# Performance work log

Measured on AMD Instinct MI355X. Metric: run time of the kernel, lower is better.

Reference implementation:

```python
import jax, jax.numpy as jnp
import numpy as np

LSTM_H = 4

def spp(x):
    # x: (N, C, H, W) -> (N, C*5) via adaptive max pool at levels [2, 1]
    N, C, H, W = x.shape
    p2 = x.reshape(N, C, 2, H // 2, 2, W // 2).max(axis=(3, 5)).reshape(N, C * 4)
    p1 = x.max(axis=(2, 3))  # (N, C)
    return jnp.concatenate([p2, p1], axis=1)  # (N, 15)

def setup_inputs() -> dict:
    key = jax.random.key(0)
    ks = jax.random.split(key, 12)
    B, S, C, H, W = 16, 128, 3, 224, 224
    s = 0.1
    return {
        "frames": jax.random.normal(ks[0], (B, S, C, H, W), dtype=jnp.float32),
        "Wf": jax.random.normal(ks[1], (15, 15), dtype=jnp.float32) * s,
        "bf": jax.random.normal(ks[2], (15,), dtype=jnp.float32) * s,
        "We": jax.random.normal(ks[3], (8, 15), dtype=jnp.float32) * s,
        "be": jax.random.normal(ks[4], (8,), dtype=jnp.float32) * s,
        "Wih": jax.random.normal(ks[5], (4 * LSTM_H, 8), dtype=jnp.float32) * s,
        "Whh": jax.random.normal(ks[6], (4 * LSTM_H, LSTM_H), dtype=jnp.float32) * s,
        "bih": jax.random.normal(ks[7], (4 * LSTM_H,), dtype=jnp.float32) * s,
        "bhh": jax.random.normal(ks[8], (4 * LSTM_H,), dtype=jnp.float32) * s,
        "Wp": jax.random.normal(ks[9], (1, LSTM_H), dtype=jnp.float32) * s,
        "bp": jax.random.normal(ks[10], (1,), dtype=jnp.float32) * s,
    }

def _lstm_cell(x, h, c, Wih, Whh, bih, bhh):
    gates = x @ Wih.T + h @ Whh.T + bih + bhh  # (B, 4H)
    i, f, g, o = jnp.split(gates, 4, axis=-1)  # torch gate order: i, f, g, o
    c2 = jax.nn.sigmoid(f) * c + jax.nn.sigmoid(i) * jnp.tanh(g)
    h2 = jax.nn.sigmoid(o) * jnp.tanh(c2)
    return h2, c2

def reference(frames, Wf, bf, We, be, Wih, Whh, bih, bhh, Wp, bp):
    B, S, C, H, W = frames.shape
    pooled_flat = spp(frames.reshape(B * S, C, H, W))          # (B*S, 15)
    forecasted_flat = pooled_flat @ Wf.T + bf                   # (B*S, 15)
    pooled = pooled_flat.reshape(B, S, 15)
    forecasted_pooled = forecasted_flat.reshape(B, S, 15)

    emb = pooled @ We.T + be                 # (B, S, 8)
    femb = forecasted_pooled @ We.T + be     # (B, S, 8)

    def step(carry, xs):
        h, c = carry
        e_t, fe_t = xs                       # each (B, 8)
        h1, c1 = _lstm_cell(e_t, h, c, Wih, Whh, bih, bhh)
        h2, _ = _lstm_cell(fe_t, h1, c1, Wih, Whh, bih, bhh)
        return (h1, c1), (h1, h2)

    h0 = jnp.zeros((B, LSTM_H), dtype=frames.dtype)
    c0 = jnp.zeros((B, LSTM_H), dtype=frames.dtype)
    xs = (jnp.swapaxes(emb, 0, 1), jnp.swapaxes(femb, 0, 1))   # (S, B, 8)
    _, (hs, fhs) = jax.lax.scan(step, (h0, c0), xs)            # (S, B, 4)

    progress = jax.nn.sigmoid(hs @ Wp.T + bp)[..., 0].T        # (B, S)
    forecasted_progress = jax.nn.sigmoid(fhs @ Wp.T + bp)[..., 0].T
    return (progress, forecasted_progress, pooled, forecasted_pooled)
```

## Files before the change

kernel.cpp:

```cpp
#include <hip/hip_runtime.h>
#include <math.h>

#define NEGINF (-INFINITY)

typedef float fvec4 __attribute__((ext_vector_type(4)));

template <int M>
__device__ __forceinline__ float qbcast(float v) {
    return __int_as_float(
        __builtin_amdgcn_update_dpp(0, __float_as_int(v), M * 0x55, 0xF, 0xF, true));
}
__device__ __forceinline__ float fsigmoid(float z) { return 1.f / (1.f + __expf(-z)); }
__device__ __forceinline__ float ftanh(float z) {
    z = fminf(fmaxf(z, -20.f), 20.f);
    float e = __expf(2.f * z);
    return (e - 1.f) / (e + 1.f);
}

__global__ __launch_bounds__(448, 7) void spp_prep_kernel(
    const float* __restrict__ frames, const float* __restrict__ Wf,
    const float* __restrict__ bf, const float* __restrict__ We,
    const float* __restrict__ be, float* __restrict__ out_pooled,
    float* __restrict__ out_fc, float* __restrict__ emb,
    float* __restrict__ femb) {
    int n = blockIdx.x;
    int tid = threadIdx.x;
    const fvec4* __restrict__ base =
        reinterpret_cast<const fvec4*>(frames) + (size_t)n * 37632;
    int cc = tid % 56;
    bool left = cc < 28;

    __shared__ float sred[7][4];
    __shared__ float sq[3][4];
    __shared__ float sp[15], sfc[15];

    for (int c = 0; c < 3; ++c) {
        const fvec4* __restrict__ p = base + c * 12544 + tid;
        float aT = NEGINF, aB = NEGINF;
#pragma unroll 7
        for (int r = 0; r < 14; ++r) {
            fvec4 f = __builtin_nontemporal_load(&p[r * 448]);
            aT = fmaxf(aT, fmaxf(fmaxf(f.x, f.y), fmaxf(f.z, f.w)));
        }
#pragma unroll 7
        for (int r = 14; r < 28; ++r) {
            fvec4 f = __builtin_nontemporal_load(&p[r * 448]);
            aB = fmaxf(aB, fmaxf(fmaxf(f.x, f.y), fmaxf(f.z, f.w)));
        }
        float tl = left ? aT : NEGINF;
        float tr = left ? NEGINF : aT;
        float bl = left ? aB : NEGINF;
        float br = left ? NEGINF : aB;
#pragma unroll
        for (int m = 32; m >= 1; m >>= 1) {
            tl = fmaxf(tl, __shfl_xor(tl, m, 64));
            tr = fmaxf(tr, __shfl_xor(tr, m, 64));
            bl = fmaxf(bl, __shfl_xor(bl, m, 64));
            br = fmaxf(br, __shfl_xor(br, m, 64));
        }
        int w = tid >> 6;
        if ((tid & 63) == 0) { sred[w][0] = tl; sred[w][1] = tr; sred[w][2] = bl; sred[w][3] = br; }
        __syncthreads();
        if (tid < 4) {
            float v = sred[0][tid];
#pragma unroll
            for (int ww = 1; ww < 7; ++ww) v = fmaxf(v, sred[ww][tid]);
            sq[c][tid] = v;
        }
        __syncthreads();
    }

    if (tid < 12) {
        sp[tid] = ((const float*)sq)[tid];
    } else if (tid >= 16 && tid < 19) {
        int c = tid - 16;
        sp[12 + c] = fmaxf(fmaxf(sq[c][0], sq[c][1]), fmaxf(sq[c][2], sq[c][3]));
    }
    __syncthreads();
    if (tid < 15) {
        float a = bf[tid];
#pragma unroll
        for (int kk = 0; kk < 15; ++kk) a += sp[kk] * Wf[tid * 15 + kk];
        sfc[tid] = a;
        out_pooled[n * 15 + tid] = sp[tid];
        out_fc[n * 15 + tid] = a;
    }
    __syncthreads();
    if (tid < 8) {
        float a = be[tid], a2 = be[tid];
#pragma unroll
        for (int kk = 0; kk < 15; ++kk) {
            a  += sp[kk]  * We[tid * 15 + kk];
            a2 += sfc[kk] * We[tid * 15 + kk];
        }
        emb[n * 8 + tid]  = a;
        femb[n * 8 + tid] = a2;
    }
}

__device__ __forceinline__ float dot8(const float4& a, const float4& b,
                                      const float* __restrict__ w) {
    return a.x * w[0] + a.y * w[1] + a.z * w[2] + a.w * w[3] +
           b.x * w[4] + b.y * w[5] + b.z * w[6] + b.w * w[7];
}

__global__ __launch_bounds__(64) void lstm_kernel(
    const float* __restrict__ emb, const float* __restrict__ femb,
    const float* __restrict__ Wih, const float* __restrict__ Whh,
    const float* __restrict__ bih, const float* __restrict__ bhh,
    const float* __restrict__ Wp, const float* __restrict__ bp,
    float* __restrict__ prog, float* __restrict__ fprog) {
    int tid = threadIdx.x;
    int b = tid >> 2, k = tid & 3;
    float wih[4][8], whh[4][4], bsum[4];
#pragma unroll
    for (int g = 0; g < 4; g++) {
        int row = g * 4 + k;
#pragma unroll
        for (int m = 0; m < 8; m++) wih[g][m] = Wih[row * 8 + m];
#pragma unroll
        for (int m = 0; m < 4; m++) whh[g][m] = Whh[row * 4 + m];
        bsum[g] = bih[row] + bhh[row];
    }
    float wpv[4];
#pragma unroll
    for (int m = 0; m < 4; m++) wpv[m] = Wp[m];
    float bpv = bp[0];

    const float* xe = emb  + b * 1024;
    const float* xf = femb + b * 1024;

    float xd1[4], xd2[4];
    {
        float4 a0 = *(const float4*)(xe);
        float4 a1 = *(const float4*)(xe + 4);
        float4 f0 = *(const float4*)(xf);
        float4 f1 = *(const float4*)(xf + 4);
#pragma unroll
        for (int g = 0; g < 4; g++) {
            xd1[g] = bsum[g] + dot8(a0, a1, wih[g]);
            xd2[g] = bsum[g] + dot8(f0, f1, wih[g]);
        }
    }

    float h0 = 0.f, h1r = 0.f, h2r = 0.f, h3r = 0.f;
    float ck = 0.f;

    for (int s2 = 0; s2 < 128; ++s2) {
        int sn = (s2 < 127) ? s2 + 1 : 127;
        float4 na0 = *(const float4*)(xe + sn * 8);
        float4 na1 = *(const float4*)(xe + sn * 8 + 4);
        float4 nf0 = *(const float4*)(xf + sn * 8);
        float4 nf1 = *(const float4*)(xf + sn * 8 + 4);

        float g0 = xd1[0] + h0 * whh[0][0] + h1r * whh[0][1] + h2r * whh[0][2] + h3r * whh[0][3];
        float g1 = xd1[1] + h0 * whh[1][0] + h1r * whh[1][1] + h2r * whh[1][2] + h3r * whh[1][3];
        float g2 = xd1[2] + h0 * whh[2][0] + h1r * whh[2][1] + h2r * whh[2][2] + h3r * whh[2][3];
        float g3 = xd1[3] + h0 * whh[3][0] + h1r * whh[3][1] + h2r * whh[3][2] + h3r * whh[3][3];
        float c1  = fsigmoid(g1) * ck + fsigmoid(g0) * ftanh(g2);
        float hk1 = fsigmoid(g3) * ftanh(c1);
        float b0 = qbcast<0>(hk1), b1 = qbcast<1>(hk1), b2 = qbcast<2>(hk1), b3 = qbcast<3>(hk1);
        float z = bpv + b0 * wpv[0] + b1 * wpv[1] + b2 * wpv[2] + b3 * wpv[3];
        if (k == 0) prog[b * 128 + s2] = fsigmoid(z);

        float e0 = xd2[0] + b0 * whh[0][0] + b1 * whh[0][1] + b2 * whh[0][2] + b3 * whh[0][3];
        float e1 = xd2[1] + b0 * whh[1][0] + b1 * whh[1][1] + b2 * whh[1][2] + b3 * whh[1][3];
        float e2 = xd2[2] + b0 * whh[2][0] + b1 * whh[2][1] + b2 * whh[2][2] + b3 * whh[2][3];
        float e3 = xd2[3] + b0 * whh[3][0] + b1 * whh[3][1] + b2 * whh[3][2] + b3 * whh[3][3];
        float c2v = fsigmoid(e1) * c1 + fsigmoid(e0) * ftanh(e2);
        float hk2 = fsigmoid(e3) * ftanh(c2v);
        float d0 = qbcast<0>(hk2), d1 = qbcast<1>(hk2), d2 = qbcast<2>(hk2), d3 = qbcast<3>(hk2);
        float z2 = bpv + d0 * wpv[0] + d1 * wpv[1] + d2 * wpv[2] + d3 * wpv[3];
        if (k == 0) fprog[b * 128 + s2] = fsigmoid(z2);

        h0 = b0; h1r = b1; h2r = b2; h3r = b3; ck = c1;

#pragma unroll
        for (int g = 0; g < 4; g++) {
            xd1[g] = bsum[g] + dot8(na0, na1, wih[g]);
            xd2[g] = bsum[g] + dot8(nf0, nf1, wih[g]);
        }
    }
}

extern "C" void kernel_launch(void* const* d_in, const int* in_sizes, int n_in,
                              void* d_out, int out_size, void* d_ws, size_t ws_size,
                              hipStream_t stream) {
    const float* frames = (const float*)d_in[0];
    const float* Wf     = (const float*)d_in[1];
    const float* bf     = (const float*)d_in[2];
    const float* We     = (const float*)d_in[3];
    const float* be     = (const float*)d_in[4];
    const float* Wih    = (const float*)d_in[5];
    const float* Whh    = (const float*)d_in[6];
    const float* bih    = (const float*)d_in[7];
    const float* bhh    = (const float*)d_in[8];
    const float* Wp     = (const float*)d_in[9];
    const float* bp     = (const float*)d_in[10];

    float* out = (float*)d_out;
    float* out_prog   = out;
    float* out_fprog  = out + 2048;
    float* out_pooled = out + 4096;
    float* out_fc     = out + 4096 + 30720;

    float* ws_f = (float*)d_ws;
    float* emb  = ws_f;
    float* femb = ws_f + 16392;

    spp_prep_kernel<<<2048, 448, 0, stream>>>(frames, Wf, bf, We, be, out_pooled,
                                              out_fc, emb, femb);
    lstm_kernel<<<1, 64, 0, stream>>>(emb, femb, Wih, Whh, bih, bhh, Wp, bp,
                                      out_prog, out_fprog);
}
```

Baseline: 288.2 us.

## Fuse SPP and LSTM into one persistent kernel with per-timestep flag pipelining

```diff
diff --git a/kernel.cpp b/kernel.cpp
--- a/kernel.cpp
+++ b/kernel.cpp
@@ -2,6 +2,8 @@
 #include <math.h>
 
 #define NEGINF (-INFINITY)
+#define AGENT __HIP_MEMORY_SCOPE_AGENT
+#define WG    __HIP_MEMORY_SCOPE_WORKGROUP
 
 typedef float fvec4 __attribute__((ext_vector_type(4)));
 
@@ -16,15 +18,129 @@
     float e = __expf(2.f * z);
     return (e - 1.f) / (e + 1.f);
 }
-
-__global__ __launch_bounds__(448, 7) void spp_prep_kernel(
+__device__ __forceinline__ float dot8(const float4& a, const float4& b,
+                                      const float* __restrict__ w) {
+    return a.x * w[0] + a.y * w[1] + a.z * w[2] + a.w * w[3] +
+           b.x * w[4] + b.y * w[5] + b.z * w[6] + b.w * w[7];
+}
+
+__global__ __launch_bounds__(448, 7) void fused_kernel(
     const float* __restrict__ frames, const float* __restrict__ Wf,
     const float* __restrict__ bf, const float* __restrict__ We,
-    const float* __restrict__ be, float* __restrict__ out_pooled,
-    float* __restrict__ out_fc, float* __restrict__ emb,
-    float* __restrict__ femb) {
-    int n = blockIdx.x;
+    const float* __restrict__ be, const float* __restrict__ Wih,
+    const float* __restrict__ Whh, const float* __restrict__ bih,
+    const float* __restrict__ bhh, const float* __restrict__ Wp,
+    const float* __restrict__ bp, float* __restrict__ out_pooled,
+    float* __restrict__ out_fc, float* __restrict__ prog,
+    float* __restrict__ fprog, int* __restrict__ cnt,
+    float* __restrict__ emb, float* __restrict__ femb) {
+    extern __shared__ float ring[];
+    __shared__ int ready[128];
+    __shared__ int consumed;
     int tid = threadIdx.x;
+
+    if (blockIdx.x == 0) {
+        for (int i = tid; i < 128; i += 448) ready[i] = 0;
+        if (tid == 0) consumed = 0;
+        __syncthreads();
+        int w = tid >> 6;
+
+        if (w == 0) {
+            int b = tid >> 2, k = tid & 3;
+            float whh_r[4][4], wpv[4];
+#pragma unroll
+            for (int g = 0; g < 4; g++) {
+                int row = g * 4 + k;
+#pragma unroll
+                for (int m = 0; m < 4; m++) whh_r[g][m] = Whh[row * 4 + m];
+            }
+#pragma unroll
+            for (int m = 0; m < 4; m++) wpv[m] = Wp[m];
+            float bpv = bp[0];
+
+            while (!__hip_atomic_load(&ready[0], __ATOMIC_ACQUIRE, WG))
+                __builtin_amdgcn_s_sleep(1);
+            float cur[8];
+#pragma unroll
+            for (int i = 0; i < 8; ++i) cur[i] = ring[i * 64 + tid];
+
+            float h0 = 0.f, h1r = 0.f, h2r = 0.f, h3r = 0.f, ck = 0.f;
+            for (int s = 0; s < 128; ++s) {
+                float g0 = cur[0] + h0 * whh_r[0][0] + h1r * whh_r[0][1] + h2r * whh_r[0][2] + h3r * whh_r[0][3];
+                float g1 = cur[1] + h0 * whh_r[1][0] + h1r * whh_r[1][1] + h2r * whh_r[1][2] + h3r * whh_r[1][3];
+                float g2 = cur[2] + h0 * whh_r[2][0] + h1r * whh_r[2][1] + h2r * whh_r[2][2] + h3r * whh_r[2][3];
+                float g3 = cur[3] + h0 * whh_r[3][0] + h1r * whh_r[3][1] + h2r * whh_r[3][2] + h3r * whh_r[3][3];
+                float c1  = fsigmoid(g1) * ck + fsigmoid(g0) * ftanh(g2);
+                float hk1 = fsigmoid(g3) * ftanh(c1);
+                float b0 = qbcast<0>(hk1), b1 = qbcast<1>(hk1), b2 = qbcast<2>(hk1), b3 = qbcast<3>(hk1);
+                float z = bpv + b0 * wpv[0] + b1 * wpv[1] + b2 * wpv[2] + b3 * wpv[3];
+                if (k == 0) prog[b * 128 + s] = fsigmoid(z);
+
+                float nxt[8];
+                if (s < 127) {
+                    while (!__hip_atomic_load(&ready[s + 1], __ATOMIC_ACQUIRE, WG))
+                        __builtin_amdgcn_s_sleep(1);
+                    int sb = ((s + 1) & 15) * 512;
+#pragma unroll
+                    for (int i = 0; i < 8; ++i) nxt[i] = ring[sb + i * 64 + tid];
+                    asm volatile("s_waitcnt lgkmcnt(0)" ::: "memory");
+                    if (tid == 0)
+                        __hip_atomic_store(&consumed, s + 2, __ATOMIC_RELEASE, WG);
+                }
+
+                float e0 = cur[4] + b0 * whh_r[0][0] + b1 * whh_r[0][1] + b2 * whh_r[0][2] + b3 * whh_r[0][3];
+                float e1 = cur[5] + b0 * whh_r[1][0] + b1 * whh_r[1][1] + b2 * whh_r[1][2] + b3 * whh_r[1][3];
+                float e2 = cur[6] + b0 * whh_r[2][0] + b1 * whh_r[2][1] + b2 * whh_r[2][2] + b3 * whh_r[2][3];
+                float e3 = cur[7] + b0 * whh_r[3][0] + b1 * whh_r[3][1] + b2 * whh_r[3][2] + b3 * whh_r[3][3];
+                float c2v = fsigmoid(e1) * c1 + fsigmoid(e0) * ftanh(e2);
+                float hk2 = fsigmoid(e3) * ftanh(c2v);
+                float d0 = qbcast<0>(hk2), d1 = qbcast<1>(hk2), d2 = qbcast<2>(hk2), d3 = qbcast<3>(hk2);
+                float z2 = bpv + d0 * wpv[0] + d1 * wpv[1] + d2 * wpv[2] + d3 * wpv[3];
+                if (k == 0) fprog[b * 128 + s] = fsigmoid(z2);
+
+                h0 = b0; h1r = b1; h2r = b2; h3r = b3; ck = c1;
+                if (s < 127) {
+#pragma unroll
+                    for (int i = 0; i < 8; ++i) cur[i] = nxt[i];
+                }
+            }
+        } else {
+            int l = tid & 63;
+            int b = l >> 2, k = l & 3;
+            float wih_r[4][8], bsum[4];
+#pragma unroll
+            for (int g = 0; g < 4; g++) {
+                int row = g * 4 + k;
+#pragma unroll
+                for (int m = 0; m < 8; m++) wih_r[g][m] = Wih[row * 8 + m];
+                bsum[g] = bih[row] + bhh[row];
+            }
+            const float* eb = emb + b * 1024;
+            const float* fb = femb + b * 1024;
+            for (int s = w - 1; s < 128; s += 6) {
+                while (__hip_atomic_load(&consumed, __ATOMIC_RELAXED, WG) < s - 15)
+                    __builtin_amdgcn_s_sleep(2);
+                while (__hip_atomic_load(&cnt[s], __ATOMIC_ACQUIRE, AGENT) < 16)
+                    __builtin_amdgcn_s_sleep(4);
+                const float4* pe = (const float4*)(eb + s * 8);
+                float4 xa = pe[0], xb = pe[1];
+                const float4* pf = (const float4*)(fb + s * 8);
+                float4 xc = pf[0], xdv = pf[1];
+                int sb = (s & 15) * 512 + l;
+#pragma unroll
+                for (int g = 0; g < 4; ++g) {
+                    ring[sb + g * 64]       = bsum[g] + dot8(xa, xb, wih_r[g]);
+                    ring[sb + (4 + g) * 64] = bsum[g] + dot8(xc, xdv, wih_r[g]);
+                }
+                asm volatile("s_waitcnt lgkmcnt(0)" ::: "memory");
+                if (l == 0)
+                    __hip_atomic_store(&ready[s], 1, __ATOMIC_RELEASE, WG);
+            }
+        }
+        return;
+    }
+
+    int n = blockIdx.x - 1;
     const fvec4* __restrict__ base =
         reinterpret_cast<const fvec4*>(frames) + (size_t)n * 37632;
     int cc = tid % 56;
@@ -93,94 +209,12 @@
             a  += sp[kk]  * We[tid * 15 + kk];
             a2 += sfc[kk] * We[tid * 15 + kk];
         }
-        emb[n * 8 + tid]  = a;
-        femb[n * 8 + tid] = a2;
-    }
-}
-
-__device__ __forceinline__ float dot8(const float4& a, const float4& b,
-                                      const float* __restrict__ w) {
-    return a.x * w[0] + a.y * w[1] + a.z * w[2] + a.w * w[3] +
-           b.x * w[4] + b.y * w[5] + b.z * w[6] + b.w * w[7];
-}
-
-__global__ __launch_bounds__(64) void lstm_kernel(
-    const float* __restrict__ emb, const float* __restrict__ femb,
-    const float* __restrict__ Wih, const float* __restrict__ Whh,
-    const float* __restrict__ bih, const float* __restrict__ bhh,
-    const float* __restrict__ Wp, const float* __restrict__ bp,
-    float* __restrict__ prog, float* __restrict__ fprog) {
-    int tid = threadIdx.x;
-    int b = tid >> 2, k = tid & 3;
-    float wih[4][8], whh[4][4], bsum[4];
-#pragma unroll
-    for (int g = 0; g < 4; g++) {
-        int row = g * 4 + k;
-#pragma unroll
-        for (int m = 0; m < 8; m++) wih[g][m] = Wih[row * 8 + m];
-#pragma unroll
-        for (int m = 0; m < 4; m++) whh[g][m] = Whh[row * 4 + m];
-        bsum[g] = bih[row] + bhh[row];
-    }
-    float wpv[4];
-#pragma unroll
-    for (int m = 0; m < 4; m++) wpv[m] = Wp[m];
-    float bpv = bp[0];
-
-    const float* xe = emb  + b * 1024;
-    const float* xf = femb + b * 1024;
-
-    float xd1[4], xd2[4];
-    {
-        float4 a0 = *(const float4*)(xe);
-        float4 a1 = *(const float4*)(xe + 4);
-        float4 f0 = *(const float4*)(xf);
-        float4 f1 = *(const float4*)(xf + 4);
-#pragma unroll
-        for (int g = 0; g < 4; g++) {
-            xd1[g] = bsum[g] + dot8(a0, a1, wih[g]);
-            xd2[g] = bsum[g] + dot8(f0, f1, wih[g]);
-        }
-    }
-
-    float h0 = 0.f, h1r = 0.f, h2r = 0.f, h3r = 0.f;
-    float ck = 0.f;
-
-    for (int s2 = 0; s2 < 128; ++s2) {
-        int sn = (s2 < 127) ? s2 + 1 : 127;
-        float4 na0 = *(const float4*)(xe + sn * 8);
-        float4 na1 = *(const float4*)(xe + sn * 8 + 4);
-        float4 nf0 = *(const float4*)(xf + sn * 8);
-        float4 nf1 = *(const float4*)(xf + sn * 8 + 4);
-
-        float g0 = xd1[0] + h0 * whh[0][0] + h1r * whh[0][1] + h2r * whh[0][2] + h3r * whh[0][3];
-        float g1 = xd1[1] + h0 * whh[1][0] + h1r * whh[1][1] + h2r * whh[1][2] + h3r * whh[1][3];
-        float g2 = xd1[2] + h0 * whh[2][0] + h1r * whh[2][1] + h2r * whh[2][2] + h3r * whh[2][3];
-        float g3 = xd1[3] + h0 * whh[3][0] + h1r * whh[3][1] + h2r * whh[3][2] + h3r * whh[3][3];
-        float c1  = fsigmoid(g1) * ck + fsigmoid(g0) * ftanh(g2);
-        float hk1 = fsigmoid(g3) * ftanh(c1);
-        float b0 = qbcast<0>(hk1), b1 = qbcast<1>(hk1), b2 = qbcast<2>(hk1), b3 = qbcast<3>(hk1);
-        float z = bpv + b0 * wpv[0] + b1 * wpv[1] + b2 * wpv[2] + b3 * wpv[3];
-        if (k == 0) prog[b * 128 + s2] = fsigmoid(z);
-
-        float e0 = xd2[0] + b0 * whh[0][0] + b1 * whh[0][1] + b2 * whh[0][2] + b3 * whh[0][3];
-        float e1 = xd2[1] + b0 * whh[1][0] + b1 * whh[1][1] + b2 * whh[1][2] + b3 * whh[1][3];
-        float e2 = xd2[2] + b0 * whh[2][0] + b1 * whh[2][1] + b2 * whh[2][2] + b3 * whh[2][3];
-        float e3 = xd2[3] + b0 * whh[3][0] + b1 * whh[3][1] + b2 * whh[3][2] + b3 * whh[3][3];
-        float c2v = fsigmoid(e1) * c1 + fsigmoid(e0) * ftanh(e2);
-        float hk2 = fsigmoid(e3) * ftanh(c2v);
-        float d0 = qbcast<0>(hk2), d1 = qbcast<1>(hk2), d2 = qbcast<2>(hk2), d3 = qbcast<3>(hk2);
-        float z2 = bpv + d0 * wpv[0] + d1 * wpv[1] + d2 * wpv[2] + d3 * wpv[3];
-        if (k == 0) fprog[b * 128 + s2] = fsigmoid(z2);
-
-        h0 = b0; h1r = b1; h2r = b2; h3r = b3; ck = c1;
-
-#pragma unroll
-        for (int g = 0; g < 4; g++) {
-            xd1[g] = bsum[g] + dot8(na0, na1, wih[g]);
-            xd2[g] = bsum[g] + dot8(nf0, nf1, wih[g]);
-        }
-    }
+        __hip_atomic_store(&emb[n * 8 + tid],  a,  __ATOMIC_RELAXED, AGENT);
+        __hip_atomic_store(&femb[n * 8 + tid], a2, __ATOMIC_RELAXED, AGENT);
+    }
+    __syncthreads();
+    if (tid == 0)
+        __hip_atomic_fetch_add(&cnt[n & 127], 1, __ATOMIC_RELEASE, AGENT);
 }
 
 extern "C" void kernel_launch(void* const* d_in, const int* in_sizes, int n_in,
@@ -204,12 +238,14 @@
     float* out_pooled = out + 4096;
     float* out_fc     = out + 4096 + 30720;
 
-    float* ws_f = (float*)d_ws;
-    float* emb  = ws_f;
-    float* femb = ws_f + 16392;
-
-    spp_prep_kernel<<<2048, 448, 0, stream>>>(frames, Wf, bf, We, be, out_pooled,
-                                              out_fc, emb, femb);
-    lstm_kernel<<<1, 64, 0, stream>>>(emb, femb, Wih, Whh, bih, bhh, Wp, bp,
-                                      out_prog, out_fprog);
-}
+    char* ws = (char*)d_ws;
+    int*   cnt  = (int*)ws;
+    float* emb  = (float*)(ws + 512);
+    float* femb = (float*)(ws + 512 + 65536);
+
+    hipMemsetAsync(cnt, 0, 128 * sizeof(int), stream);
+    fused_kernel<<<2049, 448, 32768, stream>>>(frames, Wf, bf, We, be, Wih, Whh,
+                                               bih, bhh, Wp, bp, out_pooled,
+                                               out_fc, out_prog, out_fprog,
+                                               cnt, emb, femb);
+}
```

New measurement: 361.0 us. +25.3%, slower.

## Merge SPP channel reductions, remap blocks, and split LSTM per batch with LDS

Applied to the files above, without the earlier changes.

```diff
diff --git a/kernel.cpp b/kernel.cpp
--- a/kernel.cpp
+++ b/kernel.cpp
@@ -23,58 +23,66 @@
     const float* __restrict__ be, float* __restrict__ out_pooled,
     float* __restrict__ out_fc, float* __restrict__ emb,
     float* __restrict__ femb) {
-    int n = blockIdx.x;
+    int bid = blockIdx.x;
+    int n = (bid & 7) * 256 + (bid >> 3);
     int tid = threadIdx.x;
     const fvec4* __restrict__ base =
         reinterpret_cast<const fvec4*>(frames) + (size_t)n * 37632;
     int cc = tid % 56;
     bool left = cc < 28;
 
-    __shared__ float sred[7][4];
-    __shared__ float sq[3][4];
-    __shared__ float sp[15], sfc[15];
-
+    float aT[3], aB[3];
+#pragma unroll
     for (int c = 0; c < 3; ++c) {
         const fvec4* __restrict__ p = base + c * 12544 + tid;
-        float aT = NEGINF, aB = NEGINF;
+        float t = NEGINF, bm = NEGINF;
 #pragma unroll 7
         for (int r = 0; r < 14; ++r) {
             fvec4 f = __builtin_nontemporal_load(&p[r * 448]);
-            aT = fmaxf(aT, fmaxf(fmaxf(f.x, f.y), fmaxf(f.z, f.w)));
+            t = fmaxf(t, fmaxf(fmaxf(f.x, f.y), fmaxf(f.z, f.w)));
         }
 #pragma unroll 7
         for (int r = 14; r < 28; ++r) {
             fvec4 f = __builtin_nontemporal_load(&p[r * 448]);
-            aB = fmaxf(aB, fmaxf(fmaxf(f.x, f.y), fmaxf(f.z, f.w)));
-        }
-        float tl = left ? aT : NEGINF;
-        float tr = left ? NEGINF : aT;
-        float bl = left ? aB : NEGINF;
-        float br = left ? NEGINF : aB;
-#pragma unroll
-        for (int m = 32; m >= 1; m >>= 1) {
-            tl = fmaxf(tl, __shfl_xor(tl, m, 64));
-            tr = fmaxf(tr, __shfl_xor(tr, m, 64));
-            bl = fmaxf(bl, __shfl_xor(bl, m, 64));
-            br = fmaxf(br, __shfl_xor(br, m, 64));
-        }
-        int w = tid >> 6;
-        if ((tid & 63) == 0) { sred[w][0] = tl; sred[w][1] = tr; sred[w][2] = bl; sred[w][3] = br; }
-        __syncthreads();
-        if (tid < 4) {
-            float v = sred[0][tid];
-#pragma unroll
-            for (int ww = 1; ww < 7; ++ww) v = fmaxf(v, sred[ww][tid]);
-            sq[c][tid] = v;
-        }
-        __syncthreads();
-    }
-
+            bm = fmaxf(bm, fmaxf(fmaxf(f.x, f.y), fmaxf(f.z, f.w)));
+        }
+        aT[c] = t; aB[c] = bm;
+    }
+
+    float q[12];
+#pragma unroll
+    for (int c = 0; c < 3; ++c) {
+        q[c * 4 + 0] = left ? aT[c] : NEGINF;
+        q[c * 4 + 1] = left ? NEGINF : aT[c];
+        q[c * 4 + 2] = left ? aB[c] : NEGINF;
+        q[c * 4 + 3] = left ? NEGINF : aB[c];
+    }
+#pragma unroll
+    for (int m = 32; m >= 1; m >>= 1) {
+#pragma unroll
+        for (int i = 0; i < 12; ++i) q[i] = fmaxf(q[i], __shfl_xor(q[i], m, 64));
+    }
+    __shared__ float sred[7][12];
+    __shared__ float sp[15], sfc[15];
+    int w = tid >> 6;
+    if ((tid & 63) == 0) {
+#pragma unroll
+        for (int i = 0; i < 12; ++i) sred[w][i] = q[i];
+    }
+    __syncthreads();
     if (tid < 12) {
-        sp[tid] = ((const float*)sq)[tid];
-    } else if (tid >= 16 && tid < 19) {
-        int c = tid - 16;
-        sp[12 + c] = fmaxf(fmaxf(sq[c][0], sq[c][1]), fmaxf(sq[c][2], sq[c][3]));
+        float v = sred[0][tid];
+#pragma unroll
+        for (int ww = 1; ww < 7; ++ww) v = fmaxf(v, sred[ww][tid]);
+        sp[tid] = v;
+    } else if (tid < 15) {
+        int c = tid - 12;
+        float v = NEGINF;
+#pragma unroll
+        for (int ww = 0; ww < 7; ++ww)
+#pragma unroll
+            for (int i = 0; i < 4; ++i) v = fmaxf(v, sred[ww][c * 4 + i]);
+        sp[tid] = v;
     }
     __syncthreads();
     if (tid < 15) {
@@ -110,8 +118,22 @@
     const float* __restrict__ bih, const float* __restrict__ bhh,
     const float* __restrict__ Wp, const float* __restrict__ bp,
     float* __restrict__ prog, float* __restrict__ fprog) {
+    __shared__ float le[1032], lf[1032];
     int tid = threadIdx.x;
-    int b = tid >> 2, k = tid & 3;
+    int b = blockIdx.x;
+
+    const fvec4* ge = reinterpret_cast<const fvec4*>(emb)  + b * 256;
+    const fvec4* gf = reinterpret_cast<const fvec4*>(femb) + b * 256;
+#pragma unroll
+    for (int it = 0; it < 4; ++it) {
+        int g = it * 64 + tid;
+        *reinterpret_cast<fvec4*>(&le[g * 4]) = ge[g];
+        *reinterpret_cast<fvec4*>(&lf[g * 4]) = gf[g];
+    }
+    __syncthreads();
+    if (tid >= 4) return;
+
+    int k = tid;
     float wih[4][8], whh[4][4], bsum[4];
 #pragma unroll
     for (int g = 0; g < 4; g++) {
@@ -127,15 +149,12 @@
     for (int m = 0; m < 4; m++) wpv[m] = Wp[m];
     float bpv = bp[0];
 
-    const float* xe = emb  + b * 1024;
-    const float* xf = femb + b * 1024;
-
     float xd1[4], xd2[4];
     {
-        float4 a0 = *(const float4*)(xe);
-        float4 a1 = *(const float4*)(xe + 4);
-        float4 f0 = *(const float4*)(xf);
-        float4 f1 = *(const float4*)(xf + 4);
+        float4 a0 = *(const float4*)(le);
+        float4 a1 = *(const float4*)(le + 4);
+        float4 f0 = *(const float4*)(lf);
+        float4 f1 = *(const float4*)(lf + 4);
 #pragma unroll
         for (int g = 0; g < 4; g++) {
             xd1[g] = bsum[g] + dot8(a0, a1, wih[g]);
@@ -147,11 +166,10 @@
     float ck = 0.f;
 
     for (int s2 = 0; s2 < 128; ++s2) {
-        int sn = (s2 < 127) ? s2 + 1 : 127;
-        float4 na0 = *(const float4*)(xe + sn * 8);
-        float4 na1 = *(const float4*)(xe + sn * 8 + 4);
-        float4 nf0 = *(const float4*)(xf + sn * 8);
-        float4 nf1 = *(const float4*)(xf + sn * 8 + 4);
+        float4 na0 = *(const float4*)(le + (s2 + 1) * 8);
+        float4 na1 = *(const float4*)(le + (s2 + 1) * 8 + 4);
+        float4 nf0 = *(const float4*)(lf + (s2 + 1) * 8);
+        float4 nf1 = *(const float4*)(lf + (s2 + 1) * 8 + 4);
 
         float g0 = xd1[0] + h0 * whh[0][0] + h1r * whh[0][1] + h2r * whh[0][2] + h3r * whh[0][3];
         float g1 = xd1[1] + h0 * whh[1][0] + h1r * whh[1][1] + h2r * whh[1][2] + h3r * whh[1][3];
@@ -206,10 +224,10 @@
 
     float* ws_f = (float*)d_ws;
     float* emb  = ws_f;
-    float* femb = ws_f + 16392;
+    float* femb = ws_f + 16384;
 
     spp_prep_kernel<<<2048, 448, 0, stream>>>(frames, Wf, bf, We, be, out_pooled,
                                               out_fc, emb, femb);
-    lstm_kernel<<<1, 64, 0, stream>>>(emb, femb, Wih, Whh, bih, bhh, Wp, bp,
-                                      out_prog, out_fprog);
-}
+    lstm_kernel<<<16, 64, 0, stream>>>(emb, femb, Wih, Whh, bih, bhh,
+                                       Wp, bp, out_prog, out_fprog);
+}
```

Result: slower. 305.5 us (+6.0%).
